# Kernel optimization log

Measured on AMD Instinct MI355X. Metric: run time of the kernel, lower is better.

Reference implementation:

```python
import jax, jax.numpy as jnp
import numpy as np

N_PTS = 500_000
NP_NODES = 258
L_DOMAIN = 10.0
TP = 1.0 - 1.0 / 150.0  # threshold_p
TM = 1.0 + 1.0 / 150.0  # threshold_m


def setup_inputs() -> dict:
    key = jax.random.key(0)
    k_x, _ = jax.random.split(key)
    x = jax.random.uniform(k_x, (N_PTS, 1), dtype=jnp.float32) * L_DOMAIN
    coordinates = jnp.linspace(0.0, L_DOMAIN, NP_NODES, dtype=jnp.float32)
    w_uu = jnp.ones((NP_NODES - 2,), dtype=jnp.float32)   # NodalValues_uu init
    w_dd = jnp.zeros((2,), dtype=jnp.float32)             # [u_0, u_L] = [0, 0]
    return {"x": x, "coordinates": coordinates, "w_uu": w_uu, "w_dd": w_dd}


def _hat(x, xm, xi, xp):
    # Piecewise-linear 'hat' basis: LinearBlock(left) + LinearBlock(right) + l2 bias (-1)
    left = jax.nn.relu(jax.nn.relu(xi - x) * (-1.0 / (xi - xm)) + 1.0)
    right = jax.nn.relu(jax.nn.relu(x - xi) * (-1.0 / (xp - xi)) + 1.0)
    return left + right - 1.0


def reference(x, coordinates, w_uu, w_dd):
    c = coordinates
    # Interior nodes i = 1 .. np-2 (vectorized over all shape functions)
    xm = c[:-2]          # x_{i-1}, shape [np-2]
    xi = c[1:-1]         # x_i
    xp = c[2:]           # x_{i+1}
    xi = jnp.maximum(jnp.minimum(xi, TP * xp), TM * xm)
    phi_uu = _hat(x, xm, xi, xp)          # [N, np-2] via broadcast of x [N,1]

    # Boundary shape functions (Shapefunction(-1) and Shapefunction(-2))
    xm0 = c[0] - c[-1] / 100.0
    xi0 = jnp.maximum(jnp.minimum(c[0], TP * c[1]), TM * xm0)
    xpL = c[-1] * (1.0 + 1.0 / 100.0)
    xiL = jnp.maximum(jnp.minimum(c[-1], TP * xpL), TM * c[-2])
    phi_0 = _hat(x, xm0, xi0, c[1])       # [N, 1]
    phi_L = _hat(x, c[-2], xiL, xpL)      # [N, 1]
    phi_dd = jnp.concatenate([phi_0, phi_L], axis=1)  # [N, 2]

    # InterpoLayer_uu + InterpoLayer_dd + SumLayer (weights all ones -> sum)
    u = phi_uu @ w_uu + phi_dd @ w_dd     # [N]
    return u[:, None]                     # [N, 1]
```

## Files before the change

kernel.cpp:

```cpp
#include <hip/hip_runtime.h>


#define TPf ((float)(1.0 - 1.0 / 150.0))
#define TMf ((float)(1.0 + 1.0 / 150.0))

__device__ __forceinline__ float hat_rcp(float x, float xm, float xi, float xp,
                                         float rl, float rr) {
    float l = fmaxf(fmaxf(xi - x, 0.0f) * (-rl) + 1.0f, 0.0f);
    float r = fmaxf(fmaxf(x - xi, 0.0f) * (-rr) + 1.0f, 0.0f);
    return l + r - 1.0f;
}

__global__ __launch_bounds__(256) void MeshNN_29042568855825_kernel(
    const float* __restrict__ X,
    const float* __restrict__ C,
    const float* __restrict__ Wu,
    const float* __restrict__ Wd,
    float* __restrict__ Out,
    int n)
{
    __shared__ float sc[258];
    __shared__ float sxi[256];
    __shared__ float srl[256];
    __shared__ float srr[256];
    __shared__ float sw[256];
    __shared__ float sb[12];

    const int tid = threadIdx.x;
    for (int j = tid; j < 258; j += 256) sc[j] = C[j];
    __syncthreads();

    {
        const int j = tid;
        const float xm = sc[j], xr = sc[j + 1], xp = sc[j + 2];
        const float xic = fmaxf(fminf(xr, TPf * xp), TMf * xm);
        sxi[j] = xic;
        srl[j] = 1.0f / (xic - xm);
        srr[j] = 1.0f / (xp - xic);
        sw[j]  = Wu[j];
    }
    if (tid == 0) {
        const float c0 = sc[0], c1 = sc[1], cNm2 = sc[256], cNm1 = sc[257];
        const float xm0 = c0 - cNm1 / 100.0f;
        const float xi0 = fmaxf(fminf(c0, TPf * c1), TMf * xm0);
        const float xpL = cNm1 * (float)(1.0 + 1.0 / 100.0);
        const float xiL = fmaxf(fminf(cNm1, TPf * xpL), TMf * cNm2);
        sb[0] = xm0;  sb[1] = xi0;  sb[2] = c1;
        sb[3] = 1.0f / (xi0 - xm0); sb[4] = 1.0f / (c1 - xi0);
        sb[5] = cNm2; sb[6] = xiL;  sb[7] = xpL;
        sb[8] = 1.0f / (xiL - cNm2); sb[9] = 1.0f / (xpL - xiL);
        sb[10] = Wd[0]; sb[11] = Wd[1];
    }
    __syncthreads();

    const int idx = blockIdx.x * 256 + tid;
    if (idx >= n) return;

    const float c0 = sc[0];
    const float inv_h = 257.0f / (sc[257] - c0);
    const float x = X[idx];

    int i = (int)((x - c0) * inv_h);
    i = min(max(i, 0), 256);
    while (i > 0 && x < sc[i]) --i;
    while (i < 256 && x >= sc[i + 1]) ++i;

    float u = sb[10] * hat_rcp(x, sb[0], sb[1], sb[2], sb[3], sb[4])
            + sb[11] * hat_rcp(x, sb[5], sb[6], sb[7], sb[8], sb[9]);

    if (i >= 1) {
        const int j = i - 1;
        u += sw[j] * hat_rcp(x, sc[j], sxi[j], sc[j + 2], srl[j], srr[j]);
    }
    if (i <= 255) {
        const int j = i;
        u += sw[j] * hat_rcp(x, sc[j], sxi[j], sc[j + 2], srl[j], srr[j]);
    }

    Out[idx] = u;
}

extern "C" void kernel_launch(void* const* d_in, const int* in_sizes, int n_in,
                              void* d_out, int out_size, void* d_ws, size_t ws_size,
                              hipStream_t stream) {
    const float* x  = (const float*)d_in[0];
    const float* c  = (const float*)d_in[1];
    const float* wu = (const float*)d_in[2];
    const float* wd = (const float*)d_in[3];
    float* out = (float*)d_out;

    const int n = in_sizes[0];
    const int blocks = (n + 255) / 256;
    MeshNN_29042568855825_kernel<<<blocks, 256, 0, stream>>>(x, c, wu, wd, out, n);
}
```

Baseline: 62.48 us.

## Process four points per thread with float4 loads and fewer setup barriers

```diff
diff --git a/kernel.cpp b/kernel.cpp
--- a/kernel.cpp
+++ b/kernel.cpp
@@ -26,13 +26,26 @@
     __shared__ float sw[256];
     __shared__ float sb[12];
 
-    const int tid = threadIdx.x;
-    for (int j = tid; j < 258; j += 256) sc[j] = C[j];
-    __syncthreads();
+    const int tid  = threadIdx.x;
+    const int base = (blockIdx.x * 256 + tid) * 4;
+
+    float x0 = 0.f, x1 = 0.f, x2 = 0.f, x3 = 0.f;
+    const bool full = (base + 4 <= n);
+    if (full) {
+        const float4 xv = *reinterpret_cast<const float4*>(X + base);
+        x0 = xv.x; x1 = xv.y; x2 = xv.z; x3 = xv.w;
+    } else if (base < n) {
+        x0 = X[base];
+        if (base + 1 < n) x1 = X[base + 1];
+        if (base + 2 < n) x2 = X[base + 2];
+        if (base + 3 < n) x3 = X[base + 3];
+    }
 
     {
         const int j = tid;
-        const float xm = sc[j], xr = sc[j + 1], xp = sc[j + 2];
+        const float xm = C[j], xr = C[j + 1], xp = C[j + 2];
+        sc[j] = xm;
+        if (j == 255) { sc[256] = xr; sc[257] = xp; }
         const float xic = fmaxf(fminf(xr, TPf * xp), TMf * xm);
         sxi[j] = xic;
         srl[j] = 1.0f / (xic - xm);
@@ -40,7 +53,7 @@
         sw[j]  = Wu[j];
     }
     if (tid == 0) {
-        const float c0 = sc[0], c1 = sc[1], cNm2 = sc[256], cNm1 = sc[257];
+        const float c0 = C[0], c1 = C[1], cNm2 = C[256], cNm1 = C[257];
         const float xm0 = c0 - cNm1 / 100.0f;
         const float xi0 = fmaxf(fminf(c0, TPf * c1), TMf * xm0);
         const float xpL = cNm1 * (float)(1.0 + 1.0 / 100.0);
@@ -53,31 +66,47 @@
     }
     __syncthreads();
 
-    const int idx = blockIdx.x * 256 + tid;
-    if (idx >= n) return;
+    if (base >= n) return;
 
-    const float c0 = sc[0];
+    const float c0    = sc[0];
     const float inv_h = 257.0f / (sc[257] - c0);
-    const float x = X[idx];
 
-    int i = (int)((x - c0) * inv_h);
-    i = min(max(i, 0), 256);
-    while (i > 0 && x < sc[i]) --i;
-    while (i < 256 && x >= sc[i + 1]) ++i;
+    const float bm0 = sb[0], bi0 = sb[1], bp0 = sb[2], brl0 = sb[3], brr0 = sb[4];
+    const float bmL = sb[5], biL = sb[6], bpL = sb[7], brlL = sb[8], brrL = sb[9];
+    const float wd0 = sb[10], wdL = sb[11];
 
-    float u = sb[10] * hat_rcp(x, sb[0], sb[1], sb[2], sb[3], sb[4])
-            + sb[11] * hat_rcp(x, sb[5], sb[6], sb[7], sb[8], sb[9]);
+    const float xs[4] = {x0, x1, x2, x3};
+    float out[4];
 
-    if (i >= 1) {
-        const int j = i - 1;
-        u += sw[j] * hat_rcp(x, sc[j], sxi[j], sc[j + 2], srl[j], srr[j]);
-    }
-    if (i <= 255) {
-        const int j = i;
-        u += sw[j] * hat_rcp(x, sc[j], sxi[j], sc[j + 2], srl[j], srr[j]);
+    #pragma unroll
+    for (int k = 0; k < 4; ++k) {
+        const float x = xs[k];
+
+        int i = (int)((x - c0) * inv_h);
+        i = min(max(i, 0), 256);
+        while (i > 0 && x < sc[i]) --i;
+        while (i < 256 && x >= sc[i + 1]) ++i;
+
+        float u = wd0 * hat_rcp(x, bm0, bi0, bp0, brl0, brr0)
+                + wdL * hat_rcp(x, bmL, biL, bpL, brlL, brrL);
+
+        if (i >= 1) {
+            const int j = i - 1;
+            u += sw[j] * hat_rcp(x, sc[j], sxi[j], sc[j + 2], srl[j], srr[j]);
+        }
+        if (i <= 255) {
+            const int j = i;
+            u += sw[j] * hat_rcp(x, sc[j], sxi[j], sc[j + 2], srl[j], srr[j]);
+        }
+        out[k] = u;
     }
 
-    Out[idx] = u;
+    if (full) {
+        *reinterpret_cast<float4*>(Out + base) =
+            make_float4(out[0], out[1], out[2], out[3]);
+    } else {
+        for (int k = 0; k < 4 && base + k < n; ++k) Out[base + k] = out[k];
+    }
 }
 
 extern "C" void kernel_launch(void* const* d_in, const int* in_sizes, int n_in,
@@ -90,6 +119,7 @@
     float* out = (float*)d_out;
 
     const int n = in_sizes[0];
-    const int blocks = (n + 255) / 256;
+    int blocks = (n + 1023) / 1024;
+    if (blocks < 1) blocks = 1;
     MeshNN_29042568855825_kernel<<<blocks, 256, 0, stream>>>(x, c, wu, wd, out, n);
 }
```

Result: no change. 62.36 us (-0.2%).
